# Kernel optimization log

Measured on AMD Instinct MI355X. Metric: run time of the kernel, lower is better.

The kernel has to match this reference:

```python
import jax, jax.numpy as jnp
import numpy as np

N_HEADS = 16
N_KV_HEADS = 4
N_EMBED = 2048
HEAD_DIM = 128
SECTIONS = [16, 24, 24, 16, 24, 24]


def _process_rotary(c):
    # c: [3, B, T, HEAD_DIM] -> [B, 1, T, HEAD_DIM]
    splits = np.cumsum(SECTIONS)[:-1]
    secs = jnp.split(c, splits, axis=-1)
    out = jnp.concatenate([s[i % 3] for i, s in enumerate(secs)], axis=-1)
    return out[:, None]  # add head axis


def _rotate_half(x):
    x1, x2 = jnp.split(x, 2, axis=-1)
    return jnp.concatenate([-x2, x1], axis=-1)


def setup_inputs() -> dict:
    key = jax.random.key(0)
    ks = jax.random.split(key, 12)
    B, T = 1, 2048
    s = 0.02
    return {
        "x": jax.random.normal(ks[0], (B, T, N_EMBED), jnp.float32),
        "cos": jax.random.uniform(ks[1], (3, B, T, HEAD_DIM), jnp.float32),
        "sin": jax.random.uniform(ks[2], (3, B, T, HEAD_DIM), jnp.float32),
        "Wq": jax.random.normal(ks[3], (N_EMBED, N_EMBED), jnp.float32) * s,
        "bq": jax.random.normal(ks[4], (N_EMBED,), jnp.float32) * s,
        "Wk": jax.random.normal(ks[5], (N_EMBED, N_KV_HEADS * HEAD_DIM), jnp.float32) * s,
        "bk": jax.random.normal(ks[6], (N_KV_HEADS * HEAD_DIM,), jnp.float32) * s,
        "Wv": jax.random.normal(ks[7], (N_EMBED, N_KV_HEADS * HEAD_DIM), jnp.float32) * s,
        "bv": jax.random.normal(ks[8], (N_KV_HEADS * HEAD_DIM,), jnp.float32) * s,
        "Wo": jax.random.normal(ks[9], (N_EMBED, N_EMBED), jnp.float32) * s,
    }


def reference(x, cos, sin, Wq, bq, Wk, bk, Wv, bv, Wo):
    B, T, C = x.shape
    H, Hkv, D = N_HEADS, N_KV_HEADS, HEAD_DIM
    q = (x @ Wq + bq).reshape(B, T, H, D).transpose(0, 2, 1, 3)    # [B,H,T,D]
    k = (x @ Wk + bk).reshape(B, T, Hkv, D).transpose(0, 2, 1, 3)  # [B,Hkv,T,D]
    v = (x @ Wv + bv).reshape(B, T, Hkv, D).transpose(0, 2, 1, 3)
    # multi-section rope (cos/sin are 4-dim -> custom path)
    c = _process_rotary(cos)
    s = _process_rotary(sin)
    q = q * c + _rotate_half(q) * s
    k = k * c + _rotate_half(k) * s
    present_k, present_v = k, v
    # GQA expansion (repeat_interleave over head axis)
    r = H // Hkv
    k = jnp.repeat(k, r, axis=1)
    v = jnp.repeat(v, r, axis=1)
    # causal SDPA
    scores = jnp.einsum("bhqd,bhkd->bhqk", q, k) / jnp.sqrt(jnp.float32(D))
    causal = jnp.tril(jnp.ones((T, T), dtype=bool))
    scores = jnp.where(causal, scores, jnp.finfo(scores.dtype).min)
    attn = jax.nn.softmax(scores, axis=-1)
    y = jnp.einsum("bhqk,bhkd->bhqd", attn, v)
    y = y.transpose(0, 2, 1, 3).reshape(B, T, C)
    y = y @ Wo
    return (y, present_k, present_v)
```

## Files before the change

kernel.cpp:

```cpp
#include <hip/hip_runtime.h>

typedef unsigned short u16;
typedef unsigned int u32;
typedef __attribute__((ext_vector_type(4))) float f32x4;
typedef __attribute__((ext_vector_type(8))) __bf16 bf16x8;
typedef __attribute__((ext_vector_type(4))) u16 u16x4;
typedef __attribute__((ext_vector_type(2))) u32 u32x2;


__device__ __forceinline__ u16 f2bf(float f) {
  union { float f; unsigned u; } v; v.f = f;
  unsigned r = v.u + 0x7fffu + ((v.u >> 16) & 1u);
  return (u16)(r >> 16);
}

__device__ __forceinline__ u32 pack_bf2(float a, float b) {
  union { float f; unsigned u; } x, y;
  x.f = a; y.f = b;
#if __has_builtin(__builtin_amdgcn_perm)
  return __builtin_amdgcn_perm(y.u + 0x8000u, x.u + 0x8000u, 0x07060302u);
#else
  return (u32)((x.u + 0x8000u) >> 16) | ((y.u + 0x8000u) & 0xffff0000u);
#endif
}

__device__ __forceinline__ void stage16(const void* g, void* l) {
#if __has_builtin(__builtin_amdgcn_global_load_lds)
  __builtin_amdgcn_global_load_lds((const __attribute__((address_space(1))) void*)g,
                                   (__attribute__((address_space(3))) void*)l, 16, 0, 0);
#else
  *(f32x4*)l = *(const f32x4*)g;
#endif
}

__device__ __forceinline__ f32x4 mfma16(bf16x8 a, bf16x8 b, f32x4 c) {
  return __builtin_amdgcn_mfma_f32_16x16x32_bf16(a, b, c, 0, 0, 0);
}

__device__ __forceinline__ float fexp2(float x) {
#if __has_builtin(__builtin_amdgcn_exp2f)
  return __builtin_amdgcn_exp2f(x);
#else
  return exp2f(x);
#endif
}

__device__ __forceinline__ int rope_ch(int d) {
  int dd = (d < 64) ? d : d - 64;
  return (dd < 16) ? 0 : (dd < 40 ? 1 : 2);
}


__global__ void yuna_prep(const float* __restrict__ x, u16* __restrict__ xb,
                          const float* __restrict__ cosp, const float* __restrict__ sinp,
                          float* __restrict__ csel, float* __restrict__ ssel,
                          const float* __restrict__ Wq, const float* __restrict__ Wk,
                          const float* __restrict__ Wv, const float* __restrict__ Wo,
                          u16* __restrict__ Wb, u16* __restrict__ Wob) {
  __shared__ float tile[64][65];
  const int bid = blockIdx.x;
  if (bid < 4096) {
    const int mat = bid >> 10;
    const int rem = bid & 1023;
    const float* W;
    u16* out;
    int N;
    if (mat == 0)      { W = Wq; out = Wb;                          N = 2048; }
    else if (mat == 1) { W = Wk; out = Wb + (size_t)2048 * 2048;    N = 512; }
    else if (mat == 2) { W = Wv; out = Wb + (size_t)2560 * 2048;    N = 512; }
    else               { W = Wo; out = Wob;                         N = 2048; }
    int k0 = (rem & 31) << 6, n0 = (rem >> 5) << 6;
    if (n0 >= N) return;
    int tx = threadIdx.x & 63, ty = threadIdx.x >> 6;
#pragma unroll
    for (int j = 0; j < 64; j += 4)
      tile[ty + j][tx] = W[(size_t)(k0 + ty + j) * N + n0 + tx];
    __syncthreads();
#pragma unroll
    for (int j = 0; j < 64; j += 4)
      out[(size_t)(n0 + ty + j) * 2048 + k0 + tx] = f2bf(tile[tx][ty + j]);
  } else if (bid < 8192) {
    int i = (bid - 4096) * 256 + threadIdx.x;
    f32x4 v = ((const f32x4*)x)[i];
    u16x4 o;
    o.x = f2bf(v.x); o.y = f2bf(v.y); o.z = f2bf(v.z); o.w = f2bf(v.w);
    ((u16x4*)xb)[i] = o;
  } else {
    int i = (bid - 8192) * 256 + threadIdx.x;
    int i4 = i * 4;
    int t = i4 >> 7, d = i4 & 127;
    f32x4 c, s;
#pragma unroll
    for (int j = 0; j < 4; ++j) {
      int ch = rope_ch(d + j);
      c[j] = cosp[(size_t)ch * 262144 + (size_t)t * 128 + d + j];
      s[j] = sinp[(size_t)ch * 262144 + (size_t)t * 128 + d + j];
    }
    ((f32x4*)csel)[i] = c;
    ((f32x4*)ssel)[i] = s;
  }
}

__global__ __launch_bounds__(256, 3) void yuna_gemm_qkv(
    const u16* __restrict__ A, const u16* __restrict__ Bt,
    const float* __restrict__ bq, const float* __restrict__ bk, const float* __restrict__ bv,
    const float* __restrict__ csel, const float* __restrict__ ssel,
    u16* __restrict__ qb, u16* __restrict__ kb, u16* __restrict__ vtb,
    float* __restrict__ pk, float* __restrict__ pv) {
  const int K = 2048;
  __shared__ __align__(16) char smem[49152];
  const int tid = threadIdx.x;
  const int wave = tid >> 6, lane = tid & 63;
  const int lrow = lane & 15, lkg = lane >> 4;
  const int m0 = blockIdx.x * 64;
  const int by = blockIdx.y;
  const int n0 = by * 128;
  const int sw = lrow & 7;

  const int srow = tid >> 3;
  const int ssc = (tid & 7) ^ ((tid >> 3) & 7);
  const size_t abase = (size_t)(m0 + srow) * K + ssc * 8;
  const size_t bbase = (size_t)(n0 + srow) * K + ssc * 8;

  const f32x4 fzero = {0.f, 0.f, 0.f, 0.f};
  f32x4 acc[4][2];
#pragma unroll
  for (int mi = 0; mi < 4; ++mi) { acc[mi][0] = fzero; acc[mi][1] = fzero; }

#pragma unroll
  for (int it = 0; it < 2; ++it)
    stage16(A + abase + (size_t)it * 32 * K, smem + (tid + it * 256) * 16);
#pragma unroll
  for (int it = 0; it < 4; ++it)
    stage16(Bt + bbase + (size_t)it * 32 * K, smem + 16384 + (tid + it * 256) * 16);

  for (int k0 = 0, ki = 0; k0 < K; k0 += 64, ++ki) {
    const int cur = ki & 1;
    const char* Asb = smem + cur * 8192;
    const char* Bsb = smem + 16384 + cur * 16384;
    if (k0 + 64 < K) {
      char* Asn = smem + (cur ^ 1) * 8192;
      char* Bsn = smem + 16384 + (cur ^ 1) * 16384;
#pragma unroll
      for (int it = 0; it < 2; ++it)
        stage16(A + abase + (size_t)it * 32 * K + k0 + 64, Asn + (tid + it * 256) * 16);
#pragma unroll
      for (int it = 0; it < 4; ++it)
        stage16(Bt + bbase + (size_t)it * 32 * K + k0 + 64, Bsn + (tid + it * 256) * 16);
      asm volatile("s_waitcnt vmcnt(6)\n\ts_barrier" ::: "memory");
    } else {
      asm volatile("s_waitcnt vmcnt(0)\n\ts_barrier" ::: "memory");
    }
#pragma unroll
    for (int kk = 0; kk < 2; ++kk) {
      const int cof = ((kk * 4 + lkg) ^ sw) << 4;
      bf16x8 af[4], bfr[2];
#pragma unroll
      for (int mi = 0; mi < 4; ++mi)
        af[mi] = *(const bf16x8*)(Asb + (mi * 16 + lrow) * 128 + cof);
#pragma unroll
      for (int ni = 0; ni < 2; ++ni)
        bfr[ni] = *(const bf16x8*)(Bsb + (wave * 16 + ni * 64 + lrow) * 128 + cof);
#pragma unroll
      for (int mi = 0; mi < 4; ++mi)
#pragma unroll
        for (int ni = 0; ni < 2; ++ni)
          acc[mi][ni] = mfma16(af[mi], bfr[ni], acc[mi][ni]);
    }
    asm volatile("s_barrier" ::: "memory");
  }

  if (by >= 20) {
    const int kvh = by - 20;
#pragma unroll
    for (int mi = 0; mi < 4; ++mi)
#pragma unroll
      for (int ni = 0; ni < 2; ++ni) {
        int d = wave * 16 + ni * 64 + lrow;
        float bb = bv[kvh * 128 + d];
        int mb = mi * 16 + lkg * 4;
        float v0 = acc[mi][ni][0] + bb, v1 = acc[mi][ni][1] + bb;
        float v2 = acc[mi][ni][2] + bb, v3 = acc[mi][ni][3] + bb;
        size_t pb = ((size_t)(kvh * 2048 + m0 + mb)) * 128 + d;
        pv[pb] = v0; pv[pb + 128] = v1; pv[pb + 256] = v2; pv[pb + 384] = v3;
        u16x4 w;
        w.x = f2bf(v0); w.y = f2bf(v1); w.z = f2bf(v2); w.w = f2bf(v3);
        *(u16x4*)(vtb + ((size_t)(kvh * 128 + d)) * 2048 + m0 + mb) = w;
      }
  } else {
    const float QSCALE = 1.4426950408889634f * 0.08838834764831845f;
    const bool isQ = (by < 16);
    const int h = isQ ? by : (by - 16);
    const float* bias = isQ ? bq : bk;
    const int dlo = wave * 16 + lrow;
    const float blo = bias[h * 128 + dlo];
    const float bhi = bias[h * 128 + dlo + 64];
#pragma unroll
    for (int mi = 0; mi < 4; ++mi) {
      const int tb = m0 + mi * 16 + lkg * 4;
#pragma unroll
      for (int r = 0; r < 4; ++r) {
        const int t = tb + r;
        float a = acc[mi][0][r] + blo;
        float b = acc[mi][1][r] + bhi;
        size_t cb = (size_t)t * 128 + dlo;
        float cl = csel[cb], sl = ssel[cb];
        float ch = csel[cb + 64], sh = ssel[cb + 64];
        float lo = a * cl - b * sl;
        float hi = b * ch + a * sh;
        size_t o = (((size_t)(h * 2048 + t)) << 7) + dlo;
        if (isQ) {
          qb[o] = f2bf(lo * QSCALE);
          qb[o + 64] = f2bf(hi * QSCALE);
        } else {
          kb[o] = f2bf(lo);
          kb[o + 64] = f2bf(hi);
          pk[o] = lo; pk[o + 64] = hi;
        }
      }
    }
  }
}

__global__ __launch_bounds__(256, 3) void yuna_gemm_out(
    const u16* __restrict__ A, const u16* __restrict__ Bt, float* __restrict__ C) {
  const int K = 2048;
  __shared__ __align__(16) char smem[49152];
  const int tid = threadIdx.x;
  const int wave = tid >> 6, lane = tid & 63;
  const int lrow = lane & 15, lkg = lane >> 4;
  const int m0 = blockIdx.x * 64;
  const int n0 = blockIdx.y * 128;
  const int wc = wave * 32;
  const int sw = lrow & 7;

  const int srow = tid >> 3;
  const int ssc = (tid & 7) ^ ((tid >> 3) & 7);
  const size_t abase = (size_t)(m0 + srow) * K + ssc * 8;
  const size_t bbase = (size_t)(n0 + srow) * K + ssc * 8;

  const f32x4 fzero = {0.f, 0.f, 0.f, 0.f};
  f32x4 acc[4][2];
#pragma unroll
  for (int mi = 0; mi < 4; ++mi) { acc[mi][0] = fzero; acc[mi][1] = fzero; }

#pragma unroll
  for (int it = 0; it < 2; ++it)
    stage16(A + abase + (size_t)it * 32 * K, smem + (tid + it * 256) * 16);
#pragma unroll
  for (int it = 0; it < 4; ++it)
    stage16(Bt + bbase + (size_t)it * 32 * K, smem + 16384 + (tid + it * 256) * 16);

  for (int k0 = 0, ki = 0; k0 < K; k0 += 64, ++ki) {
    const int cur = ki & 1;
    const char* Asb = smem + cur * 8192;
    const char* Bsb = smem + 16384 + cur * 16384;
    if (k0 + 64 < K) {
      char* Asn = smem + (cur ^ 1) * 8192;
      char* Bsn = smem + 16384 + (cur ^ 1) * 16384;
#pragma unroll
      for (int it = 0; it < 2; ++it)
        stage16(A + abase + (size_t)it * 32 * K + k0 + 64, Asn + (tid + it * 256) * 16);
#pragma unroll
      for (int it = 0; it < 4; ++it)
        stage16(Bt + bbase + (size_t)it * 32 * K + k0 + 64, Bsn + (tid + it * 256) * 16);
      asm volatile("s_waitcnt vmcnt(6)\n\ts_barrier" ::: "memory");
    } else {
      asm volatile("s_waitcnt vmcnt(0)\n\ts_barrier" ::: "memory");
    }
#pragma unroll
    for (int kk = 0; kk < 2; ++kk) {
      const int cof = ((kk * 4 + lkg) ^ sw) << 4;
      bf16x8 af[4], bfr[2];
#pragma unroll
      for (int mi = 0; mi < 4; ++mi)
        af[mi] = *(const bf16x8*)(Asb + (mi * 16 + lrow) * 128 + cof);
#pragma unroll
      for (int ni = 0; ni < 2; ++ni)
        bfr[ni] = *(const bf16x8*)(Bsb + (wc + ni * 16 + lrow) * 128 + cof);
#pragma unroll
      for (int mi = 0; mi < 4; ++mi)
#pragma unroll
        for (int ni = 0; ni < 2; ++ni)
          acc[mi][ni] = mfma16(af[mi], bfr[ni], acc[mi][ni]);
    }
    asm volatile("s_barrier" ::: "memory");
  }
#pragma unroll
  for (int mi = 0; mi < 4; ++mi)
#pragma unroll
    for (int ni = 0; ni < 2; ++ni) {
      int d = wc + ni * 16 + lrow;
      int mb = mi * 16 + lkg * 4;
#pragma unroll
      for (int r = 0; r < 4; ++r)
        C[(size_t)(m0 + mb + r) * 2048 + n0 + d] = acc[mi][ni][r];
    }
}

__global__ __launch_bounds__(256, 2) void yuna_flash_attn(
    const u16* __restrict__ Q,
    const u16* __restrict__ Kb,
    const u16* __restrict__ Vt,
    u16* __restrict__ Y) {
  __shared__ __align__(16) u16 Ks[2][64 * 128];
  __shared__ __align__(16) u16 Vs[2][128 * 64];
  __shared__ __align__(16) u16 Ps[64 * 64];
  const int h = blockIdx.x;
  const int yb = blockIdx.y;
  const int qb = (yb & 1) ? (yb >> 1) : 31 - (yb >> 1);
  const int kvh = h >> 2;
  const int tid = threadIdx.x, wave = tid >> 6, lane = tid & 63;
  const int lrow = lane & 15, lkg = lane >> 4;
  const int m = wave * 16 + lrow;
  const int sw = lrow & 7;

  const int krow = tid >> 4;
  const int ksc = (tid & 15) ^ ((tid >> 4) & 7);
  const size_t kbase0 = ((size_t)(kvh * 2048 + krow) << 7) + ksc * 8;
  const int vrow = tid >> 3;
  const int vsc = (tid & 7) ^ ((tid >> 3) & 7);
  const size_t vbase0 = (size_t)(kvh * 128 + vrow) * 2048 + vsc * 8;

  bf16x8 qf[4];
#pragma unroll
  for (int kk = 0; kk < 4; ++kk)
    qf[kk] = *(const bf16x8*)(Q + (((size_t)h * 2048 + qb * 64 + m) << 7) + kk * 32 + lkg * 8);

  const f32x4 fzero = {0.f, 0.f, 0.f, 0.f};
  f32x4 o[8];
#pragma unroll
  for (int dt = 0; dt < 8; ++dt) o[dt] = fzero;
  float m_i = -1e30f, l_i = 0.f;

  const int nkb = qb + 1;

#pragma unroll
  for (int it = 0; it < 4; ++it)
    stage16(Kb + kbase0 + ((size_t)(it * 16) << 7), (char*)Ks[0] + (tid + it * 256) * 16);
#pragma unroll
  for (int it = 0; it < 4; ++it)
    stage16(Vt + vbase0 + (size_t)it * 32 * 2048, (char*)Vs[0] + (tid + it * 256) * 16);

  for (int kb = 0; kb < nkb; ++kb) {
    const int cur = kb & 1;
    const char* Ksb = (const char*)Ks[cur];
    const char* Vsb = (const char*)Vs[cur];
    if (kb + 1 < nkb) {
      char* Ksn = (char*)Ks[cur ^ 1];
      char* Vsn = (char*)Vs[cur ^ 1];
#pragma unroll
      for (int it = 0; it < 4; ++it)
        stage16(Kb + kbase0 + ((size_t)((kb + 1) * 64 + it * 16) << 7), Ksn + (tid + it * 256) * 16);
#pragma unroll
      for (int it = 0; it < 4; ++it)
        stage16(Vt + vbase0 + (size_t)it * 32 * 2048 + (kb + 1) * 64, Vsn + (tid + it * 256) * 16);
      asm volatile("s_waitcnt vmcnt(8)\n\ts_barrier" ::: "memory");
    } else {
      asm volatile("s_waitcnt vmcnt(0)\n\ts_barrier" ::: "memory");
    }

    f32x4 s[4];
#pragma unroll
    for (int nt = 0; nt < 4; ++nt) s[nt] = fzero;
    __builtin_amdgcn_s_setprio(1);
#pragma unroll
    for (int kk = 0; kk < 4; ++kk) {
      const int cof = ((kk * 4 + lkg) ^ sw) << 4;
      bf16x8 kf[4];
#pragma unroll
      for (int nt = 0; nt < 4; ++nt)
        kf[nt] = *(const bf16x8*)(Ksb + (nt * 16 + lrow) * 256 + cof);
#pragma unroll
      for (int nt = 0; nt < 4; ++nt)
        s[nt] = mfma16(kf[nt], qf[kk], s[nt]);
    }
    __builtin_amdgcn_s_setprio(0);
    if (kb == qb) {
#pragma unroll
      for (int nt = 0; nt < 4; ++nt)
#pragma unroll
        for (int r = 0; r < 4; ++r)
          if (nt * 16 + lkg * 4 + r > m) s[nt][r] = -1e30f;
    }

    float mx = -1e30f;
#pragma unroll
    for (int nt = 0; nt < 4; ++nt)
#pragma unroll
      for (int r = 0; r < 4; ++r) mx = fmaxf(mx, s[nt][r]);
    mx = fmaxf(mx, __shfl_xor(mx, 16));
    mx = fmaxf(mx, __shfl_xor(mx, 32));
    if (__any(mx > m_i + 8.0f)) {
      float mnew = fmaxf(m_i, mx);
      float alpha = fexp2(m_i - mnew);
      m_i = mnew;
      l_i *= alpha;
#pragma unroll
      for (int dt = 0; dt < 8; ++dt) o[dt] *= alpha;
    }
    float ps = 0.f;
    const int hh = lkg & 1;
#pragma unroll
    for (int nt = 0; nt < 4; ++nt) {
      float p0 = fexp2(s[nt][0] - m_i);
      float p1 = fexp2(s[nt][1] - m_i);
      float p2 = fexp2(s[nt][2] - m_i);
      float p3 = fexp2(s[nt][3] - m_i);
      ps += (p0 + p1) + (p2 + p3);
      u32x2 pk2;
      pk2.x = pack_bf2(p0, p1);
      pk2.y = pack_bf2(p2, p3);
      int cc = 2 * nt + (lkg >> 1);
      *(u32x2*)((char*)Ps + m * 128 + ((cc ^ (m & 7)) << 4) + hh * 8) = pk2;
    }
    ps += __shfl_xor(ps, 16);
    ps += __shfl_xor(ps, 32);
    l_i += ps;

    __builtin_amdgcn_s_setprio(1);
#pragma unroll
    for (int kk = 0; kk < 2; ++kk) {
      const int cof = ((kk * 4 + lkg) ^ sw) << 4;
      bf16x8 pf = *(const bf16x8*)((char*)Ps + m * 128 + cof);
      bf16x8 vf[8];
#pragma unroll
      for (int dt = 0; dt < 8; ++dt)
        vf[dt] = *(const bf16x8*)(Vsb + (dt * 16 + lrow) * 128 + cof);
#pragma unroll
      for (int dt = 0; dt < 8; ++dt)
        o[dt] = mfma16(vf[dt], pf, o[dt]);
    }
    __builtin_amdgcn_s_setprio(0);
    asm volatile("s_barrier" ::: "memory");
  }

  __syncthreads();
  {
    float inv = 1.f / l_i;
    const int hh = lkg & 1;
#pragma unroll
    for (int dt = 0; dt < 8; ++dt) {
      u32x2 w2;
      w2.x = pack_bf2(o[dt][0] * inv, o[dt][1] * inv);
      w2.y = pack_bf2(o[dt][2] * inv, o[dt][3] * inv);
      int cc = 2 * dt + (lkg >> 1);
      *(u32x2*)((char*)Ks[0] + m * 256 + ((cc ^ (m & 7)) << 4) + hh * 8) = w2;
    }
  }
  __syncthreads();
#pragma unroll
  for (int it = 0; it < 4; ++it) {
    int c = tid + it * 256;
    int row = c >> 4, cc = c & 15;
    f32x4 v = *(const f32x4*)((const char*)Ks[0] + row * 256 + ((cc ^ (row & 7)) << 4));
    *(f32x4*)(Y + (size_t)(qb * 64 + row) * 2048 + h * 128 + cc * 8) = v;
  }
}


extern "C" void kernel_launch(void* const* d_in, const int* in_sizes, int n_in,
                              void* d_out, int out_size, void* d_ws, size_t ws_size,
                              hipStream_t stream) {
  const float* x = (const float*)d_in[0];
  const float* cosp = (const float*)d_in[1];
  const float* sinp = (const float*)d_in[2];
  const float* Wq = (const float*)d_in[3];
  const float* bq = (const float*)d_in[4];
  const float* Wk = (const float*)d_in[5];
  const float* bk = (const float*)d_in[6];
  const float* Wv = (const float*)d_in[7];
  const float* bv = (const float*)d_in[8];
  const float* Wo = (const float*)d_in[9];
  float* out = (float*)d_out;
  float* out_k = out + 4194304;
  float* out_v = out + 5242880;

  char* ws = (char*)d_ws;
  u16* xb   = (u16*)(ws + 0);
  u16* Wb   = (u16*)(ws + 8388608);
  u16* Wob  = (u16*)(ws + 20971520);
  float* csel = (float*)(ws + 29360128);
  float* ssel = (float*)(ws + 30408704);
  u16* qbuf = (u16*)(ws + 54525952);
  u16* kbuf = (u16*)(ws + 62914560);
  u16* vtb  = (u16*)(ws + 65011712);
  u16* yat  = (u16*)(ws + 67108864);

  yuna_prep<<<8448, 256, 0, stream>>>(x, xb, cosp, sinp, csel, ssel,
                                      Wq, Wk, Wv, Wo, Wb, Wob);
  yuna_gemm_qkv<<<dim3(32, 24), 256, 0, stream>>>(xb, Wb, bq, bk, bv, csel, ssel,
                                                  qbuf, kbuf, vtb, out_k, out_v);
  yuna_flash_attn<<<dim3(16, 32), 256, 0, stream>>>(qbuf, kbuf, vtb, yat);
  yuna_gemm_out<<<dim3(32, 16), 256, 0, stream>>>(yat, Wob, out);
}
```

Before: 221.4 us.

## Widen attention KV tiles to 128 and read V fragments straight from global

The flash-attention kernel now handles 128 keys per iteration instead of 64, so it runs half as many loop trips and barriers per query block. V is no longer staged in LDS: each lane loads its V fragments directly from global memory inside the PV MFMA loop, and the P tile and its swizzle are widened to match. The causal mask now uses absolute key and query positions, the query-block ordering across the grid changes, and the row-max reduction becomes a vector tree. The trade-off is that V reads are strided 16-byte global loads with no prefetch, so they depend on L2 and expose latency. Half of the last 128-key tile is masked work for even query blocks.

```diff
diff --git a/kernel.cpp b/kernel.cpp
--- a/kernel.cpp
+++ b/kernel.cpp
@@ -43,6 +43,13 @@
 #else
   return exp2f(x);
 #endif
+}
+
+__device__ __forceinline__ f32x4 max4(f32x4 a, f32x4 b) {
+  f32x4 r;
+  r[0] = fmaxf(a[0], b[0]); r[1] = fmaxf(a[1], b[1]);
+  r[2] = fmaxf(a[2], b[2]); r[3] = fmaxf(a[3], b[3]);
+  return r;
 }
 
 __device__ __forceinline__ int rope_ch(int d) {
@@ -303,24 +310,23 @@
     const u16* __restrict__ Kb,
     const u16* __restrict__ Vt,
     u16* __restrict__ Y) {
-  __shared__ __align__(16) u16 Ks[2][64 * 128];
-  __shared__ __align__(16) u16 Vs[2][128 * 64];
-  __shared__ __align__(16) u16 Ps[64 * 64];
+  __shared__ __align__(16) u16 Ks[2][128 * 128];
+  __shared__ __align__(16) u16 Ps[64 * 128];
   const int h = blockIdx.x;
   const int yb = blockIdx.y;
-  const int qb = (yb & 1) ? (yb >> 1) : 31 - (yb >> 1);
+  const int qb = (yb < 16) ? yb : 47 - yb;
   const int kvh = h >> 2;
   const int tid = threadIdx.x, wave = tid >> 6, lane = tid & 63;
   const int lrow = lane & 15, lkg = lane >> 4;
   const int m = wave * 16 + lrow;
   const int sw = lrow & 7;
+  const int qglob = qb * 64 + m;
 
   const int krow = tid >> 4;
   const int ksc = (tid & 15) ^ ((tid >> 4) & 7);
   const size_t kbase0 = ((size_t)(kvh * 2048 + krow) << 7) + ksc * 8;
-  const int vrow = tid >> 3;
-  const int vsc = (tid & 7) ^ ((tid >> 3) & 7);
-  const size_t vbase0 = (size_t)(kvh * 128 + vrow) * 2048 + vsc * 8;
+
+  const u16* vbase = Vt + (size_t)(kvh * 128 + lrow) * 2048 + lkg * 8;
 
   bf16x8 qf[4];
 #pragma unroll
@@ -333,62 +339,54 @@
   for (int dt = 0; dt < 8; ++dt) o[dt] = fzero;
   float m_i = -1e30f, l_i = 0.f;
 
-  const int nkb = qb + 1;
-
-#pragma unroll
-  for (int it = 0; it < 4; ++it)
+  const int nkb = (qb >> 1) + 1;
+
+#pragma unroll
+  for (int it = 0; it < 8; ++it)
     stage16(Kb + kbase0 + ((size_t)(it * 16) << 7), (char*)Ks[0] + (tid + it * 256) * 16);
-#pragma unroll
-  for (int it = 0; it < 4; ++it)
-    stage16(Vt + vbase0 + (size_t)it * 32 * 2048, (char*)Vs[0] + (tid + it * 256) * 16);
 
   for (int kb = 0; kb < nkb; ++kb) {
     const int cur = kb & 1;
     const char* Ksb = (const char*)Ks[cur];
-    const char* Vsb = (const char*)Vs[cur];
     if (kb + 1 < nkb) {
       char* Ksn = (char*)Ks[cur ^ 1];
-      char* Vsn = (char*)Vs[cur ^ 1];
-#pragma unroll
-      for (int it = 0; it < 4; ++it)
-        stage16(Kb + kbase0 + ((size_t)((kb + 1) * 64 + it * 16) << 7), Ksn + (tid + it * 256) * 16);
-#pragma unroll
-      for (int it = 0; it < 4; ++it)
-        stage16(Vt + vbase0 + (size_t)it * 32 * 2048 + (kb + 1) * 64, Vsn + (tid + it * 256) * 16);
+#pragma unroll
+      for (int it = 0; it < 8; ++it)
+        stage16(Kb + kbase0 + ((size_t)((kb + 1) * 128 + it * 16) << 7), Ksn + (tid + it * 256) * 16);
       asm volatile("s_waitcnt vmcnt(8)\n\ts_barrier" ::: "memory");
     } else {
       asm volatile("s_waitcnt vmcnt(0)\n\ts_barrier" ::: "memory");
     }
 
-    f32x4 s[4];
-#pragma unroll
-    for (int nt = 0; nt < 4; ++nt) s[nt] = fzero;
+    f32x4 s[8];
+#pragma unroll
+    for (int nt = 0; nt < 8; ++nt) s[nt] = fzero;
     __builtin_amdgcn_s_setprio(1);
 #pragma unroll
     for (int kk = 0; kk < 4; ++kk) {
       const int cof = ((kk * 4 + lkg) ^ sw) << 4;
-      bf16x8 kf[4];
-#pragma unroll
-      for (int nt = 0; nt < 4; ++nt)
+      bf16x8 kf[8];
+#pragma unroll
+      for (int nt = 0; nt < 8; ++nt)
         kf[nt] = *(const bf16x8*)(Ksb + (nt * 16 + lrow) * 256 + cof);
 #pragma unroll
-      for (int nt = 0; nt < 4; ++nt)
+      for (int nt = 0; nt < 8; ++nt)
         s[nt] = mfma16(kf[nt], qf[kk], s[nt]);
     }
     __builtin_amdgcn_s_setprio(0);
-    if (kb == qb) {
-#pragma unroll
-      for (int nt = 0; nt < 4; ++nt)
+    if (kb == nkb - 1) {
+      const int kbase = kb * 128 + lkg * 4;
+#pragma unroll
+      for (int nt = 0; nt < 8; ++nt)
 #pragma unroll
         for (int r = 0; r < 4; ++r)
-          if (nt * 16 + lkg * 4 + r > m) s[nt][r] = -1e30f;
-    }
-
-    float mx = -1e30f;
-#pragma unroll
-    for (int nt = 0; nt < 4; ++nt)
-#pragma unroll
-      for (int r = 0; r < 4; ++r) mx = fmaxf(mx, s[nt][r]);
+          if (kbase + nt * 16 + r > qglob) s[nt][r] = -1e30f;
+    }
+
+    f32x4 t01 = max4(s[0], s[1]), t23 = max4(s[2], s[3]);
+    f32x4 t45 = max4(s[4], s[5]), t67 = max4(s[6], s[7]);
+    f32x4 ta = max4(max4(t01, t23), max4(t45, t67));
+    float mx = fmaxf(fmaxf(ta[0], ta[1]), fmaxf(ta[2], ta[3]));
     mx = fmaxf(mx, __shfl_xor(mx, 16));
     mx = fmaxf(mx, __shfl_xor(mx, 32));
     if (__any(mx > m_i + 8.0f)) {
@@ -402,7 +400,7 @@
     float ps = 0.f;
     const int hh = lkg & 1;
 #pragma unroll
-    for (int nt = 0; nt < 4; ++nt) {
+    for (int nt = 0; nt < 8; ++nt) {
       float p0 = fexp2(s[nt][0] - m_i);
       float p1 = fexp2(s[nt][1] - m_i);
       float p2 = fexp2(s[nt][2] - m_i);
@@ -412,24 +410,28 @@
       pk2.x = pack_bf2(p0, p1);
       pk2.y = pack_bf2(p2, p3);
       int cc = 2 * nt + (lkg >> 1);
-      *(u32x2*)((char*)Ps + m * 128 + ((cc ^ (m & 7)) << 4) + hh * 8) = pk2;
+      *(u32x2*)((char*)Ps + m * 256 + (((cc ^ (m & 15))) << 4) + hh * 8) = pk2;
     }
     ps += __shfl_xor(ps, 16);
     ps += __shfl_xor(ps, 32);
     l_i += ps;
 
+    bf16x8 pf[4];
+#pragma unroll
+    for (int ks = 0; ks < 4; ++ks)
+      pf[ks] = *(const bf16x8*)((char*)Ps + m * 256 + ((((ks * 4 + lkg) ^ (m & 15))) << 4));
+    const u16* vb = vbase + kb * 128;
     __builtin_amdgcn_s_setprio(1);
 #pragma unroll
-    for (int kk = 0; kk < 2; ++kk) {
-      const int cof = ((kk * 4 + lkg) ^ sw) << 4;
-      bf16x8 pf = *(const bf16x8*)((char*)Ps + m * 128 + cof);
-      bf16x8 vf[8];
-#pragma unroll
-      for (int dt = 0; dt < 8; ++dt)
-        vf[dt] = *(const bf16x8*)(Vsb + (dt * 16 + lrow) * 128 + cof);
-#pragma unroll
-      for (int dt = 0; dt < 8; ++dt)
-        o[dt] = mfma16(vf[dt], pf, o[dt]);
+    for (int dt = 0; dt < 8; ++dt) {
+      bf16x8 vf0 = *(const bf16x8*)(vb + (size_t)(dt * 16) * 2048);
+      bf16x8 vf1 = *(const bf16x8*)(vb + (size_t)(dt * 16) * 2048 + 32);
+      bf16x8 vf2 = *(const bf16x8*)(vb + (size_t)(dt * 16) * 2048 + 64);
+      bf16x8 vf3 = *(const bf16x8*)(vb + (size_t)(dt * 16) * 2048 + 96);
+      o[dt] = mfma16(vf0, pf[0], o[dt]);
+      o[dt] = mfma16(vf1, pf[1], o[dt]);
+      o[dt] = mfma16(vf2, pf[2], o[dt]);
+      o[dt] = mfma16(vf3, pf[3], o[dt]);
     }
     __builtin_amdgcn_s_setprio(0);
     asm volatile("s_barrier" ::: "memory");
```

After: 272.3 us. 23.0% more time.

## Shrink flash-attention KV tile to 32 rows to raise occupancy to four blocks

Applied to the files above, without the earlier changes.

The flash-attention kernel now streams K/V in 32-key tiles instead of 64, halving the shared-memory footprint of the K, V and P buffers. Launch bounds move from two to four blocks per CU. The V shared-memory layout and swizzle are reworked for 64-byte rows, and the P buffer gets a padded 80-byte row stride. The query-block ordering and causal masking are adapted to the finer tiles. The aim is more latency hiding through higher occupancy, at the cost of more barriers and loop iterations per query block, fewer MFMAs per sync, and a tighter register budget that could cause spills.

```diff
diff --git a/kernel.cpp b/kernel.cpp
--- a/kernel.cpp
+++ b/kernel.cpp
@@ -298,28 +298,30 @@
     }
 }
 
-__global__ __launch_bounds__(256, 2) void yuna_flash_attn(
+__global__ __launch_bounds__(256, 4) void yuna_flash_attn(
     const u16* __restrict__ Q,
     const u16* __restrict__ Kb,
     const u16* __restrict__ Vt,
     u16* __restrict__ Y) {
-  __shared__ __align__(16) u16 Ks[2][64 * 128];
-  __shared__ __align__(16) u16 Vs[2][128 * 64];
-  __shared__ __align__(16) u16 Ps[64 * 64];
+  __shared__ __align__(16) u16 Ks[2][32 * 128];
+  __shared__ __align__(16) u16 Vs[2][128 * 32];
+  __shared__ __align__(16) u16 Ps[64 * 40];
   const int h = blockIdx.x;
   const int yb = blockIdx.y;
-  const int qb = (yb & 1) ? (yb >> 1) : 31 - (yb >> 1);
+  const int qb = (yb < 16) ? yb : 47 - yb;
   const int kvh = h >> 2;
   const int tid = threadIdx.x, wave = tid >> 6, lane = tid & 63;
   const int lrow = lane & 15, lkg = lane >> 4;
   const int m = wave * 16 + lrow;
   const int sw = lrow & 7;
+  const int qglob = qb * 64 + m;
 
   const int krow = tid >> 4;
   const int ksc = (tid & 15) ^ ((tid >> 4) & 7);
   const size_t kbase0 = ((size_t)(kvh * 2048 + krow) << 7) + ksc * 8;
-  const int vrow = tid >> 3;
-  const int vsc = (tid & 7) ^ ((tid >> 3) & 7);
+
+  const int vrow = tid >> 2;
+  const int vsc = (tid & 3) ^ ((vrow ^ (vrow >> 2)) & 3);
   const size_t vbase0 = (size_t)(kvh * 128 + vrow) * 2048 + vsc * 8;
 
   bf16x8 qf[4];
@@ -333,14 +335,14 @@
   for (int dt = 0; dt < 8; ++dt) o[dt] = fzero;
   float m_i = -1e30f, l_i = 0.f;
 
-  const int nkb = qb + 1;
-
-#pragma unroll
-  for (int it = 0; it < 4; ++it)
+  const int nkb = 2 * qb + 2;
+
+#pragma unroll
+  for (int it = 0; it < 2; ++it)
     stage16(Kb + kbase0 + ((size_t)(it * 16) << 7), (char*)Ks[0] + (tid + it * 256) * 16);
 #pragma unroll
-  for (int it = 0; it < 4; ++it)
-    stage16(Vt + vbase0 + (size_t)it * 32 * 2048, (char*)Vs[0] + (tid + it * 256) * 16);
+  for (int it = 0; it < 2; ++it)
+    stage16(Vt + vbase0 + (size_t)it * 64 * 2048, (char*)Vs[0] + (tid + it * 256) * 16);
 
   for (int kb = 0; kb < nkb; ++kb) {
     const int cur = kb & 1;
@@ -350,43 +352,40 @@
       char* Ksn = (char*)Ks[cur ^ 1];
       char* Vsn = (char*)Vs[cur ^ 1];
 #pragma unroll
-      for (int it = 0; it < 4; ++it)
-        stage16(Kb + kbase0 + ((size_t)((kb + 1) * 64 + it * 16) << 7), Ksn + (tid + it * 256) * 16);
-#pragma unroll
-      for (int it = 0; it < 4; ++it)
-        stage16(Vt + vbase0 + (size_t)it * 32 * 2048 + (kb + 1) * 64, Vsn + (tid + it * 256) * 16);
-      asm volatile("s_waitcnt vmcnt(8)\n\ts_barrier" ::: "memory");
+      for (int it = 0; it < 2; ++it)
+        stage16(Kb + kbase0 + ((size_t)((kb + 1) * 32 + it * 16) << 7), Ksn + (tid + it * 256) * 16);
+#pragma unroll
+      for (int it = 0; it < 2; ++it)
+        stage16(Vt + vbase0 + (size_t)it * 64 * 2048 + (kb + 1) * 32, Vsn + (tid + it * 256) * 16);
+      asm volatile("s_waitcnt vmcnt(4)\n\ts_barrier" ::: "memory");
     } else {
       asm volatile("s_waitcnt vmcnt(0)\n\ts_barrier" ::: "memory");
     }
 
-    f32x4 s[4];
-#pragma unroll
-    for (int nt = 0; nt < 4; ++nt) s[nt] = fzero;
+    f32x4 s[2];
+    s[0] = fzero; s[1] = fzero;
     __builtin_amdgcn_s_setprio(1);
 #pragma unroll
     for (int kk = 0; kk < 4; ++kk) {
       const int cof = ((kk * 4 + lkg) ^ sw) << 4;
-      bf16x8 kf[4];
-#pragma unroll
-      for (int nt = 0; nt < 4; ++nt)
-        kf[nt] = *(const bf16x8*)(Ksb + (nt * 16 + lrow) * 256 + cof);
-#pragma unroll
-      for (int nt = 0; nt < 4; ++nt)
-        s[nt] = mfma16(kf[nt], qf[kk], s[nt]);
+      bf16x8 kf0 = *(const bf16x8*)(Ksb + (lrow) * 256 + cof);
+      bf16x8 kf1 = *(const bf16x8*)(Ksb + (16 + lrow) * 256 + cof);
+      s[0] = mfma16(kf0, qf[kk], s[0]);
+      s[1] = mfma16(kf1, qf[kk], s[1]);
     }
     __builtin_amdgcn_s_setprio(0);
-    if (kb == qb) {
-#pragma unroll
-      for (int nt = 0; nt < 4; ++nt)
+    if (kb >= 2 * qb) {
+      const int kbase = kb * 32 + lkg * 4;
+#pragma unroll
+      for (int nt = 0; nt < 2; ++nt)
 #pragma unroll
         for (int r = 0; r < 4; ++r)
-          if (nt * 16 + lkg * 4 + r > m) s[nt][r] = -1e30f;
+          if (kbase + nt * 16 + r > qglob) s[nt][r] = -1e30f;
     }
 
     float mx = -1e30f;
 #pragma unroll
-    for (int nt = 0; nt < 4; ++nt)
+    for (int nt = 0; nt < 2; ++nt)
 #pragma unroll
       for (int r = 0; r < 4; ++r) mx = fmaxf(mx, s[nt][r]);
     mx = fmaxf(mx, __shfl_xor(mx, 16));
@@ -400,9 +399,8 @@
       for (int dt = 0; dt < 8; ++dt) o[dt] *= alpha;
     }
     float ps = 0.f;
-    const int hh = lkg & 1;
-#pragma unroll
-    for (int nt = 0; nt < 4; ++nt) {
+#pragma unroll
+    for (int nt = 0; nt < 2; ++nt) {
       float p0 = fexp2(s[nt][0] - m_i);
       float p1 = fexp2(s[nt][1] - m_i);
       float p2 = fexp2(s[nt][2] - m_i);
@@ -411,25 +409,19 @@
       u32x2 pk2;
       pk2.x = pack_bf2(p0, p1);
       pk2.y = pack_bf2(p2, p3);
-      int cc = 2 * nt + (lkg >> 1);
-      *(u32x2*)((char*)Ps + m * 128 + ((cc ^ (m & 7)) << 4) + hh * 8) = pk2;
+      *(u32x2*)((char*)Ps + m * 80 + nt * 32 + lkg * 8) = pk2;
     }
     ps += __shfl_xor(ps, 16);
     ps += __shfl_xor(ps, 32);
     l_i += ps;
 
+    bf16x8 pf = *(const bf16x8*)((char*)Ps + m * 80 + lkg * 16);
+    const int vch = (lkg ^ ((lrow ^ (lrow >> 2)) & 3)) << 4;
     __builtin_amdgcn_s_setprio(1);
 #pragma unroll
-    for (int kk = 0; kk < 2; ++kk) {
-      const int cof = ((kk * 4 + lkg) ^ sw) << 4;
-      bf16x8 pf = *(const bf16x8*)((char*)Ps + m * 128 + cof);
-      bf16x8 vf[8];
-#pragma unroll
-      for (int dt = 0; dt < 8; ++dt)
-        vf[dt] = *(const bf16x8*)(Vsb + (dt * 16 + lrow) * 128 + cof);
-#pragma unroll
-      for (int dt = 0; dt < 8; ++dt)
-        o[dt] = mfma16(vf[dt], pf, o[dt]);
+    for (int dt = 0; dt < 8; ++dt) {
+      bf16x8 vf = *(const bf16x8*)(Vsb + (dt * 16 + lrow) * 64 + vch);
+      o[dt] = mfma16(vf, pf, o[dt]);
     }
     __builtin_amdgcn_s_setprio(0);
     asm volatile("s_barrier" ::: "memory");
@@ -445,7 +437,7 @@
       w2.x = pack_bf2(o[dt][0] * inv, o[dt][1] * inv);
       w2.y = pack_bf2(o[dt][2] * inv, o[dt][3] * inv);
       int cc = 2 * dt + (lkg >> 1);
-      *(u32x2*)((char*)Ks[0] + m * 256 + ((cc ^ (m & 7)) << 4) + hh * 8) = w2;
+      *(u32x2*)((char*)Ks + m * 256 + ((cc ^ (m & 7)) << 4) + hh * 8) = w2;
     }
   }
   __syncthreads();
@@ -453,7 +445,7 @@
   for (int it = 0; it < 4; ++it) {
     int c = tid + it * 256;
     int row = c >> 4, cc = c & 15;
-    f32x4 v = *(const f32x4*)((const char*)Ks[0] + row * 256 + ((cc ^ (row & 7)) << 4));
+    f32x4 v = *(const f32x4*)((const char*)Ks + row * 256 + ((cc ^ (row & 7)) << 4));
     *(f32x4*)(Y + (size_t)(qb * 64 + row) * 2048 + h * 128 + cc * 8) = v;
   }
 }
```

Result: slower. 240.2 us (+8.5%).

## Split causal attention KV range in two and merge partial results

Applied to the files above, without the earlier changes.

Each query block's causal KV range is split into two halves handled by separate workgroups, doubling the attention grid. Each half writes unnormalized fp32 partial outputs plus per-row max and sum. A new merge kernel combines the halves into the bf16 attention output. The aim is better load balance and more parallelism across CUs, and the per-iteration row-sum shuffle is deferred to the end. The cost is an extra kernel launch and tens of MB of fp32 partial-output traffic, with buffers reusing dead workspace regions.

```diff
diff --git a/kernel.cpp b/kernel.cpp
--- a/kernel.cpp
+++ b/kernel.cpp
@@ -302,18 +302,25 @@
     const u16* __restrict__ Q,
     const u16* __restrict__ Kb,
     const u16* __restrict__ Vt,
-    u16* __restrict__ Y) {
+    float* __restrict__ OpA,
+    float* __restrict__ OpB,
+    float* __restrict__ ml) {
   __shared__ __align__(16) u16 Ks[2][64 * 128];
   __shared__ __align__(16) u16 Vs[2][128 * 64];
   __shared__ __align__(16) u16 Ps[64 * 64];
   const int h = blockIdx.x;
   const int yb = blockIdx.y;
-  const int qb = (yb & 1) ? (yb >> 1) : 31 - (yb >> 1);
+  const int qb = 31 - (yb >> 1);
+  const int half = yb & 1;
+  const int ca = (qb + 2) >> 1;
+  const int kb0 = half ? ca : 0;
+  const int kb1 = half ? (qb + 1) : ca;
   const int kvh = h >> 2;
   const int tid = threadIdx.x, wave = tid >> 6, lane = tid & 63;
   const int lrow = lane & 15, lkg = lane >> 4;
   const int m = wave * 16 + lrow;
   const int sw = lrow & 7;
+  const int qglob = qb * 64 + m;
 
   const int krow = tid >> 4;
   const int ksc = (tid & 15) ^ ((tid >> 4) & 7);
@@ -325,7 +332,7 @@
   bf16x8 qf[4];
 #pragma unroll
   for (int kk = 0; kk < 4; ++kk)
-    qf[kk] = *(const bf16x8*)(Q + (((size_t)h * 2048 + qb * 64 + m) << 7) + kk * 32 + lkg * 8);
+    qf[kk] = *(const bf16x8*)(Q + (((size_t)h * 2048 + qglob) << 7) + kk * 32 + lkg * 8);
 
   const f32x4 fzero = {0.f, 0.f, 0.f, 0.f};
   f32x4 o[8];
@@ -333,129 +340,139 @@
   for (int dt = 0; dt < 8; ++dt) o[dt] = fzero;
   float m_i = -1e30f, l_i = 0.f;
 
-  const int nkb = qb + 1;
-
-#pragma unroll
-  for (int it = 0; it < 4; ++it)
-    stage16(Kb + kbase0 + ((size_t)(it * 16) << 7), (char*)Ks[0] + (tid + it * 256) * 16);
-#pragma unroll
-  for (int it = 0; it < 4; ++it)
-    stage16(Vt + vbase0 + (size_t)it * 32 * 2048, (char*)Vs[0] + (tid + it * 256) * 16);
-
-  for (int kb = 0; kb < nkb; ++kb) {
-    const int cur = kb & 1;
-    const char* Ksb = (const char*)Ks[cur];
-    const char* Vsb = (const char*)Vs[cur];
-    if (kb + 1 < nkb) {
-      char* Ksn = (char*)Ks[cur ^ 1];
-      char* Vsn = (char*)Vs[cur ^ 1];
-#pragma unroll
-      for (int it = 0; it < 4; ++it)
-        stage16(Kb + kbase0 + ((size_t)((kb + 1) * 64 + it * 16) << 7), Ksn + (tid + it * 256) * 16);
-#pragma unroll
-      for (int it = 0; it < 4; ++it)
-        stage16(Vt + vbase0 + (size_t)it * 32 * 2048 + (kb + 1) * 64, Vsn + (tid + it * 256) * 16);
-      asm volatile("s_waitcnt vmcnt(8)\n\ts_barrier" ::: "memory");
-    } else {
-      asm volatile("s_waitcnt vmcnt(0)\n\ts_barrier" ::: "memory");
-    }
-
-    f32x4 s[4];
-#pragma unroll
-    for (int nt = 0; nt < 4; ++nt) s[nt] = fzero;
-    __builtin_amdgcn_s_setprio(1);
-#pragma unroll
-    for (int kk = 0; kk < 4; ++kk) {
-      const int cof = ((kk * 4 + lkg) ^ sw) << 4;
-      bf16x8 kf[4];
+  if (kb0 < kb1) {
+#pragma unroll
+    for (int it = 0; it < 4; ++it)
+      stage16(Kb + kbase0 + ((size_t)(kb0 * 64 + it * 16) << 7), (char*)Ks[0] + (tid + it * 256) * 16);
+#pragma unroll
+    for (int it = 0; it < 4; ++it)
+      stage16(Vt + vbase0 + (size_t)it * 32 * 2048 + kb0 * 64, (char*)Vs[0] + (tid + it * 256) * 16);
+
+    for (int kb = kb0; kb < kb1; ++kb) {
+      const int cur = (kb - kb0) & 1;
+      const char* Ksb = (const char*)Ks[cur];
+      const char* Vsb = (const char*)Vs[cur];
+      if (kb + 1 < kb1) {
+        char* Ksn = (char*)Ks[cur ^ 1];
+        char* Vsn = (char*)Vs[cur ^ 1];
+#pragma unroll
+        for (int it = 0; it < 4; ++it)
+          stage16(Kb + kbase0 + ((size_t)((kb + 1) * 64 + it * 16) << 7), Ksn + (tid + it * 256) * 16);
+#pragma unroll
+        for (int it = 0; it < 4; ++it)
+          stage16(Vt + vbase0 + (size_t)it * 32 * 2048 + (kb + 1) * 64, Vsn + (tid + it * 256) * 16);
+        asm volatile("s_waitcnt vmcnt(8)\n\ts_barrier" ::: "memory");
+      } else {
+        asm volatile("s_waitcnt vmcnt(0)\n\ts_barrier" ::: "memory");
+      }
+
+      f32x4 s[4];
+#pragma unroll
+      for (int nt = 0; nt < 4; ++nt) s[nt] = fzero;
+      __builtin_amdgcn_s_setprio(1);
+#pragma unroll
+      for (int kk = 0; kk < 4; ++kk) {
+        const int cof = ((kk * 4 + lkg) ^ sw) << 4;
+        bf16x8 kf[4];
+#pragma unroll
+        for (int nt = 0; nt < 4; ++nt)
+          kf[nt] = *(const bf16x8*)(Ksb + (nt * 16 + lrow) * 256 + cof);
+#pragma unroll
+        for (int nt = 0; nt < 4; ++nt)
+          s[nt] = mfma16(kf[nt], qf[kk], s[nt]);
+      }
+      __builtin_amdgcn_s_setprio(0);
+      if (kb == qb) {
+        const int kbase = kb * 64 + lkg * 4;
+#pragma unroll
+        for (int nt = 0; nt < 4; ++nt)
+#pragma unroll
+          for (int r = 0; r < 4; ++r)
+            if (kbase + nt * 16 + r > qglob) s[nt][r] = -1e30f;
+      }
+
+      float mx = -1e30f;
 #pragma unroll
       for (int nt = 0; nt < 4; ++nt)
-        kf[nt] = *(const bf16x8*)(Ksb + (nt * 16 + lrow) * 256 + cof);
-#pragma unroll
-      for (int nt = 0; nt < 4; ++nt)
-        s[nt] = mfma16(kf[nt], qf[kk], s[nt]);
-    }
-    __builtin_amdgcn_s_setprio(0);
-    if (kb == qb) {
-#pragma unroll
-      for (int nt = 0; nt < 4; ++nt)
-#pragma unroll
-        for (int r = 0; r < 4; ++r)
-          if (nt * 16 + lkg * 4 + r > m) s[nt][r] = -1e30f;
-    }
-
-    float mx = -1e30f;
-#pragma unroll
-    for (int nt = 0; nt < 4; ++nt)
-#pragma unroll
-      for (int r = 0; r < 4; ++r) mx = fmaxf(mx, s[nt][r]);
-    mx = fmaxf(mx, __shfl_xor(mx, 16));
-    mx = fmaxf(mx, __shfl_xor(mx, 32));
-    if (__any(mx > m_i + 8.0f)) {
-      float mnew = fmaxf(m_i, mx);
-      float alpha = fexp2(m_i - mnew);
-      m_i = mnew;
-      l_i *= alpha;
-#pragma unroll
-      for (int dt = 0; dt < 8; ++dt) o[dt] *= alpha;
-    }
-    float ps = 0.f;
-    const int hh = lkg & 1;
-#pragma unroll
-    for (int nt = 0; nt < 4; ++nt) {
-      float p0 = fexp2(s[nt][0] - m_i);
-      float p1 = fexp2(s[nt][1] - m_i);
-      float p2 = fexp2(s[nt][2] - m_i);
-      float p3 = fexp2(s[nt][3] - m_i);
-      ps += (p0 + p1) + (p2 + p3);
-      u32x2 pk2;
-      pk2.x = pack_bf2(p0, p1);
-      pk2.y = pack_bf2(p2, p3);
-      int cc = 2 * nt + (lkg >> 1);
-      *(u32x2*)((char*)Ps + m * 128 + ((cc ^ (m & 7)) << 4) + hh * 8) = pk2;
-    }
-    ps += __shfl_xor(ps, 16);
-    ps += __shfl_xor(ps, 32);
-    l_i += ps;
-
-    __builtin_amdgcn_s_setprio(1);
-#pragma unroll
-    for (int kk = 0; kk < 2; ++kk) {
-      const int cof = ((kk * 4 + lkg) ^ sw) << 4;
-      bf16x8 pf = *(const bf16x8*)((char*)Ps + m * 128 + cof);
-      bf16x8 vf[8];
-#pragma unroll
-      for (int dt = 0; dt < 8; ++dt)
-        vf[dt] = *(const bf16x8*)(Vsb + (dt * 16 + lrow) * 128 + cof);
-#pragma unroll
-      for (int dt = 0; dt < 8; ++dt)
-        o[dt] = mfma16(vf[dt], pf, o[dt]);
-    }
-    __builtin_amdgcn_s_setprio(0);
-    asm volatile("s_barrier" ::: "memory");
+#pragma unroll
+        for (int r = 0; r < 4; ++r) mx = fmaxf(mx, s[nt][r]);
+      mx = fmaxf(mx, __shfl_xor(mx, 16));
+      mx = fmaxf(mx, __shfl_xor(mx, 32));
+      if (__any(mx > m_i + 8.0f)) {
+        float mnew = fmaxf(m_i, mx);
+        float alpha = fexp2(m_i - mnew);
+        m_i = mnew;
+        l_i *= alpha;
+#pragma unroll
+        for (int dt = 0; dt < 8; ++dt) o[dt] *= alpha;
+      }
+      float ps = 0.f;
+      const int hh = lkg & 1;
+#pragma unroll
+      for (int nt = 0; nt < 4; ++nt) {
+        float p0 = fexp2(s[nt][0] - m_i);
+        float p1 = fexp2(s[nt][1] - m_i);
+        float p2 = fexp2(s[nt][2] - m_i);
+        float p3 = fexp2(s[nt][3] - m_i);
+        ps += (p0 + p1) + (p2 + p3);
+        u32x2 pk2;
+        pk2.x = pack_bf2(p0, p1);
+        pk2.y = pack_bf2(p2, p3);
+        int cc = 2 * nt + (lkg >> 1);
+        *(u32x2*)((char*)Ps + m * 128 + ((cc ^ (m & 7)) << 4) + hh * 8) = pk2;
+      }
+      l_i += ps;
+
+      __builtin_amdgcn_s_setprio(1);
+#pragma unroll
+      for (int kk = 0; kk < 2; ++kk) {
+        const int cof = ((kk * 4 + lkg) ^ sw) << 4;
+        bf16x8 pf = *(const bf16x8*)((char*)Ps + m * 128 + cof);
+        bf16x8 vf[8];
+#pragma unroll
+        for (int dt = 0; dt < 8; ++dt)
+          vf[dt] = *(const bf16x8*)(Vsb + (dt * 16 + lrow) * 128 + cof);
+#pragma unroll
+        for (int dt = 0; dt < 8; ++dt)
+          o[dt] = mfma16(vf[dt], pf, o[dt]);
+      }
+      __builtin_amdgcn_s_setprio(0);
+      asm volatile("s_barrier" ::: "memory");
+    }
   }
 
-  __syncthreads();
-  {
-    float inv = 1.f / l_i;
-    const int hh = lkg & 1;
-#pragma unroll
-    for (int dt = 0; dt < 8; ++dt) {
-      u32x2 w2;
-      w2.x = pack_bf2(o[dt][0] * inv, o[dt][1] * inv);
-      w2.y = pack_bf2(o[dt][2] * inv, o[dt][3] * inv);
-      int cc = 2 * dt + (lkg >> 1);
-      *(u32x2*)((char*)Ks[0] + m * 256 + ((cc ^ (m & 7)) << 4) + hh * 8) = w2;
-    }
-  }
-  __syncthreads();
-#pragma unroll
-  for (int it = 0; it < 4; ++it) {
-    int c = tid + it * 256;
-    int row = c >> 4, cc = c & 15;
-    f32x4 v = *(const f32x4*)((const char*)Ks[0] + row * 256 + ((cc ^ (row & 7)) << 4));
-    *(f32x4*)(Y + (size_t)(qb * 64 + row) * 2048 + h * 128 + cc * 8) = v;
-  }
+  l_i += __shfl_xor(l_i, 16);
+  l_i += __shfl_xor(l_i, 32);
+  size_t row = (size_t)h * 2048 + qglob;
+  if (lkg == 0)
+    *(float2*)(ml + ((size_t)(half << 15) + row) * 2) = float2{m_i, l_i};
+  float* orow = (half ? OpB : OpA) + row * 128 + lkg * 4;
+#pragma unroll
+  for (int dt = 0; dt < 8; ++dt)
+    *(f32x4*)(orow + dt * 16) = o[dt];
+}
+
+__global__ void yuna_merge(const float* __restrict__ OpA, const float* __restrict__ OpB,
+                           const float* __restrict__ ml, u16* __restrict__ Y) {
+  int idx = blockIdx.x * 256 + threadIdx.x;
+  int d4 = idx & 31;
+  int t = (idx >> 5) & 2047;
+  int h = idx >> 16;
+  size_t row = (size_t)h * 2048 + t;
+  float2 a2 = *(const float2*)(ml + row * 2);
+  float2 b2 = *(const float2*)(ml + (32768 + row) * 2);
+  float M = fmaxf(a2.x, b2.x);
+  float wA = fexp2(a2.x - M), wB = fexp2(b2.x - M);
+  float inv = 1.f / (a2.y * wA + b2.y * wB);
+  wA *= inv; wB *= inv;
+  f32x4 a = ((const f32x4*)OpA)[row * 32 + d4];
+  f32x4 b = ((const f32x4*)OpB)[row * 32 + d4];
+  u16x4 w;
+  w.x = f2bf(a[0] * wA + b[0] * wB);
+  w.y = f2bf(a[1] * wA + b[1] * wB);
+  w.z = f2bf(a[2] * wA + b[2] * wB);
+  w.w = f2bf(a[3] * wA + b[3] * wB);
+  *(u16x4*)(Y + (size_t)t * 2048 + h * 128 + d4 * 4) = w;
 }
 
 
@@ -486,11 +503,15 @@
   u16* kbuf = (u16*)(ws + 62914560);
   u16* vtb  = (u16*)(ws + 65011712);
   u16* yat  = (u16*)(ws + 67108864);
+  float* opA = (float*)(ws + 0);
+  float* mlb = (float*)(ws + 17825792);
+  float* opB = (float*)(ws + 31457280);
 
   yuna_prep<<<8448, 256, 0, stream>>>(x, xb, cosp, sinp, csel, ssel,
                                       Wq, Wk, Wv, Wo, Wb, Wob);
   yuna_gemm_qkv<<<dim3(32, 24), 256, 0, stream>>>(xb, Wb, bq, bk, bv, csel, ssel,
                                                   qbuf, kbuf, vtb, out_k, out_v);
-  yuna_flash_attn<<<dim3(16, 32), 256, 0, stream>>>(qbuf, kbuf, vtb, yat);
+  yuna_flash_attn<<<dim3(16, 64), 256, 0, stream>>>(qbuf, kbuf, vtb, opA, opB, mlb);
+  yuna_merge<<<4096, 256, 0, stream>>>(opA, opB, mlb, yat);
   yuna_gemm_out<<<dim3(32, 16), 256, 0, stream>>>(yat, Wob, out);
 }
```

New measurement: 216.9 us. 1.02x faster.
